# Kernel optimization log

Measured on AMD Instinct MI355X. Metric: run time of the kernel, lower is better.

The kernel has to match this reference:

```python
import jax, jax.numpy as jnp
import numpy as np

B, S, D, H = 2, 2048, 1024, 16
DK = D // H  # 64


def setup_inputs() -> dict:
    key = jax.random.key(0)
    k0, k1, k2, k3, k4, k5, k6 = jax.random.split(key, 7)
    scale = 0.02
    return {
        "q": jax.random.normal(k0, (B, S, D), dtype=jnp.float32),
        "k": jax.random.normal(k1, (B, S, D), dtype=jnp.float32),
        "v": jax.random.normal(k2, (B, S, D), dtype=jnp.float32),
        # per-head Q/K projection weights (n_head separate Linear layers, bias=False)
        "Wq": jax.random.normal(k3, (H, D, DK), dtype=jnp.float32) * scale,
        "Wk": jax.random.normal(k4, (H, D, DK), dtype=jnp.float32) * scale,
        # shared V projection (the same v_layer object is reused for every head)
        "Wv": jax.random.normal(k5, (D, DK), dtype=jnp.float32) * scale,
        # output projection fc: d_v -> d_model, bias=False
        "Wo": jax.random.normal(k6, (DK, D), dtype=jnp.float32) * scale,
    }


def reference(q, k, v, Wq, Wk, Wv, Wo):
    d_k = Wq.shape[-1]
    # batched per-head projections (replaces the Python loop over heads)
    qs = jnp.einsum("bsd,hdk->bhsk", q, Wq)          # [B,H,S,DK]
    ks = jnp.einsum("bsd,hdk->bhsk", k, Wk)          # [B,H,S,DK]
    vs = jnp.einsum("bsd,dk->bsk", v, Wv)            # [B,S,DK] shared across heads
    scores = jnp.einsum("bhsk,bhtk->bhst", qs, ks) / jnp.sqrt(
        jnp.asarray(d_k, dtype=jnp.float32)
    )                                                 # [B,H,S,S]
    attn = jax.nn.softmax(scores, axis=-1)            # [B,H,S,S]; dropout = identity (eval)
    heads = jnp.einsum("bhst,btk->bhsk", attn, vs)    # [B,H,S,DK]
    head = heads.mean(axis=1)                         # mean over heads, not concat
    attn_mean = attn.mean(axis=1)                     # [B,S,S]
    out = jnp.einsum("bsk,kd->bsd", head, Wo)         # [B,S,D]; dropout = identity
    return (out, attn_mean)
```

## Files before the change

kernel.cpp:

```cpp
#include <hip/hip_runtime.h>

#define B_ 2
#define S_ 2048
#define D_ 1024
#define H_ 16
#define DK_ 64

typedef __bf16 bf8 __attribute__((ext_vector_type(8)));
typedef float f4 __attribute__((ext_vector_type(4)));
typedef unsigned short u16x8 __attribute__((ext_vector_type(8)));

__device__ __forceinline__ unsigned short f2bf_bits(float f) {
  unsigned int u = __float_as_uint(f);
  return (unsigned short)((u + 0x7fffu + ((u >> 16) & 1u)) >> 16);
}

__device__ __forceinline__ bf8 pack_bf8(f4 lo, f4 hi) {
  u16x8 u;
  u[0] = f2bf_bits(lo[0]); u[1] = f2bf_bits(lo[1]);
  u[2] = f2bf_bits(lo[2]); u[3] = f2bf_bits(lo[3]);
  u[4] = f2bf_bits(hi[0]); u[5] = f2bf_bits(hi[1]);
  u[6] = f2bf_bits(hi[2]); u[7] = f2bf_bits(hi[3]);
  union { u16x8 u; bf8 b; } x; x.u = u; return x.b;
}

__device__ __forceinline__ bf8 ldb(const unsigned short* p) {
  return *reinterpret_cast<const bf8*>(p);
}

__device__ __forceinline__ void stage16(const void* g, void* l) {
  __builtin_amdgcn_global_load_lds(
      (const __attribute__((address_space(1))) void*)g,
      (__attribute__((address_space(3))) void*)l, 16, 0, 0);
}

#define MFMA(a, b, c) __builtin_amdgcn_mfma_f32_16x16x32_bf16((a), (b), (c), 0, 0, 0)

__global__ void k_prep(const float* __restrict__ q, const float* __restrict__ k,
                       const float* __restrict__ wq, const float* __restrict__ wk,
                       const float* __restrict__ wv, const float* __restrict__ wo,
                       unsigned short* __restrict__ qb, unsigned short* __restrict__ kb,
                       unsigned short* __restrict__ wqt, unsigned short* __restrict__ wkt,
                       unsigned short* __restrict__ wvt, unsigned short* __restrict__ wot) {
  int bid = blockIdx.x, tid = threadIdx.x;
  if (bid < 4096) {
    int which = bid >> 11;
    long i = ((long)(bid & 2047) * 256 + tid) * 8;
    const float* src = which ? k : q;
    unsigned short* dst = which ? kb : qb;
    f4 lo = *reinterpret_cast<const f4*>(src + i);
    f4 hi = *reinterpret_cast<const f4*>(src + i + 4);
    *reinterpret_cast<bf8*>(dst + i) = pack_bf8(lo, hi);
  } else if (bid < 8192) {
    int i = (bid - 4096) * 256 + tid;
    int h = i >> 16, rem = i & 65535, n = rem >> 10, d = rem & 1023;
    long src = ((long)h << 16) + d * 64 + n;
    wqt[i] = f2bf_bits(wq[src]);
    wkt[i] = f2bf_bits(wk[src]);
  } else {
    int i = (bid - 8192) * 256 + tid;
    int n = i >> 10, d = i & 1023;
    wvt[i] = f2bf_bits(wv[d * 64 + n]);
    int dd = i >> 6, kk = i & 63;
    wot[i] = f2bf_bits(wo[kk * 1024 + dd]);
  }
}

__global__ __launch_bounds__(256) void k_gemm_qk(
    const unsigned short* __restrict__ qb, const unsigned short* __restrict__ kb,
    const unsigned short* __restrict__ wqt, const unsigned short* __restrict__ wkt,
    unsigned short* __restrict__ qsb, unsigned short* __restrict__ ksb) {
  __shared__ unsigned short lds[6144];
  const int tid = threadIdx.x, wave = tid >> 6, lane = tid & 63;
  const int l15 = lane & 15, quad = lane >> 4;
  const int m0 = blockIdx.x * 128, n0 = blockIdx.y * 64;
  const int which = blockIdx.z;
  const unsigned short* A = which ? kb : qb;
  const unsigned short* W = which ? wkt : wqt;
  unsigned short* C = which ? ksb : qsb;
  const float scale = which ? 1.0f : 0.18033688011112042f;
  const int wr = wave >> 1, wc = wave & 1;

  f4 acc[4][2];
#pragma unroll
  for (int i = 0; i < 4; ++i)
#pragma unroll
    for (int j = 0; j < 2; ++j) acc[i][j] = f4{0.f, 0.f, 0.f, 0.f};

  const int sl15 = tid & 15, squad = (tid >> 4) & 3, sT = tid >> 6;

  for (int k0 = 0; k0 < D_; k0 += 32) {
    stage16(A + (long)(m0 + sT * 16 + sl15) * D_ + k0 + squad * 8, lds + tid * 8);
    stage16(A + (long)(m0 + 64 + sT * 16 + sl15) * D_ + k0 + squad * 8, lds + 2048 + tid * 8);
    stage16(W + (long)(n0 + sT * 16 + sl15) * D_ + k0 + squad * 8, lds + 4096 + tid * 8);
    __syncthreads();
    bf8 aF[4], bF[2];
#pragma unroll
    for (int mi = 0; mi < 4; ++mi)
      aF[mi] = ldb(lds + (wr * 4 + mi) * 512 + lane * 8);
#pragma unroll
    for (int ni = 0; ni < 2; ++ni)
      bF[ni] = ldb(lds + 4096 + (wc * 2 + ni) * 512 + lane * 8);
#pragma unroll
    for (int mi = 0; mi < 4; ++mi)
#pragma unroll
      for (int ni = 0; ni < 2; ++ni)
        acc[mi][ni] = MFMA(aF[mi], bF[ni], acc[mi][ni]);
    __syncthreads();
  }
#pragma unroll
  for (int mi = 0; mi < 4; ++mi)
#pragma unroll
    for (int r = 0; r < 4; ++r) {
      long row = m0 + wr * 64 + mi * 16 + quad * 4 + r;
#pragma unroll
      for (int ni = 0; ni < 2; ++ni)
        C[row * D_ + n0 + wc * 32 + ni * 16 + l15] = f2bf_bits(acc[mi][ni][r] * scale);
    }
}

__global__ __launch_bounds__(256) void k_pv(
    const float* __restrict__ v, const unsigned short* __restrict__ wvt,
    float* __restrict__ pv) {
  const int tid = threadIdx.x, wave = tid >> 6, lane = tid & 63;
  const int l15 = lane & 15, quad = lane >> 4;
  const int rg = blockIdx.x, kc = blockIdx.y;
  const int row0 = rg * 64 + wave * 16;
  const float* arow = v + (long)(row0 + l15) * D_ + kc * 256 + quad * 8;
  const unsigned short* wbase = wvt + kc * 256 + quad * 8;
  f4 acc[4];
  for (int i = 0; i < 4; ++i) acc[i] = f4{0.f, 0.f, 0.f, 0.f};
  for (int k0 = 0; k0 < 256; k0 += 32) {
    f4 alo = *reinterpret_cast<const f4*>(arow + k0);
    f4 ahi = *reinterpret_cast<const f4*>(arow + k0 + 4);
    bf8 a = pack_bf8(alo, ahi);
#pragma unroll
    for (int i = 0; i < 4; ++i) {
      bf8 bf = ldb(wbase + (long)(i * 16 + l15) * D_ + k0);
      acc[i] = MFMA(a, bf, acc[i]);
    }
  }
#pragma unroll
  for (int i = 0; i < 4; ++i)
#pragma unroll
    for (int r = 0; r < 4; ++r)
      pv[((long)kc * 4096 + row0 + quad * 4 + r) * 64 + i * 16 + l15] = acc[i][r];
}

__global__ void k_vred(const float* __restrict__ pv, unsigned short* __restrict__ vst) {
  int e = blockIdx.x * 256 + threadIdx.x;
  int t = e & 2047, dk = (e >> 11) & 63, b = e >> 17;
  long row = (long)b * S_ + t;
  float s = pv[row * 64 + dk] + pv[(4096 + row) * 64 + dk] +
            pv[(8192 + row) * 64 + dk] + pv[(12288 + row) * 64 + dk];
  vst[e] = f2bf_bits(s);
}

__global__ __launch_bounds__(1024) void k_denom(
    const unsigned short* __restrict__ qsb, const unsigned short* __restrict__ ksb,
    float* __restrict__ recip) {
  __shared__ unsigned short lds[8192];
  const int tid = threadIdx.x, wave = tid >> 6, lane = tid & 63;
  const int l15 = lane & 15, quad = lane >> 4;
  const int stile = blockIdx.x, h = blockIdx.y, b = blockIdx.z;
  const int s0 = stile * 256 + wave * 16;

  const unsigned short* qrow = qsb + ((long)(b * S_) + s0 + l15) * D_ + h * 64 + quad * 8;
  bf8 a0 = ldb(qrow);
  bf8 a1 = ldb(qrow + 32);

  const int sl15 = tid & 15, squad = (tid >> 4) & 3, stt = (tid >> 6) & 7, sh2 = tid >> 9;
  const unsigned short* gsrc0 =
      ksb + ((long)(b * S_) + stt * 16 + sl15) * D_ + h * 64 + sh2 * 32 + squad * 8;

  f4 sum = f4{0.f, 0.f, 0.f, 0.f};
  for (int t0 = 0; t0 < S_; t0 += 128) {
    stage16(gsrc0 + (long)t0 * D_, lds + tid * 8);
    __syncthreads();
#pragma unroll
    for (int tt = 0; tt < 8; ++tt) {
      bf8 b0 = ldb(lds + tt * 512 + lane * 8);
      bf8 b1 = ldb(lds + 4096 + tt * 512 + lane * 8);
      f4 d = f4{0.f, 0.f, 0.f, 0.f};
      d = MFMA(a0, b0, d);
      d = MFMA(a1, b1, d);
#pragma unroll
      for (int r = 0; r < 4; ++r) sum[r] += __builtin_amdgcn_exp2f(d[r]);
    }
    __syncthreads();
  }
#pragma unroll
  for (int m = 1; m < 16; m <<= 1) {
#pragma unroll
    for (int r = 0; r < 4; ++r) sum[r] += __shfl_xor(sum[r], m, 64);
  }
  if (l15 == 0) {
    float* rp = recip + (long)(b * H_ + h) * S_ + s0 + quad * 4;
#pragma unroll
    for (int r = 0; r < 4; ++r) rp[r] = 1.0f / (16.0f * sum[r]);
  }
}

__global__ __launch_bounds__(512) void k_attn(
    const unsigned short* __restrict__ qsb, const unsigned short* __restrict__ ksb,
    const float* __restrict__ recip, float* __restrict__ am) {
  __shared__ unsigned short lds[8192];
  const int tid = threadIdx.x, wave = tid >> 6, lane = tid & 63;
  const int l15 = lane & 15, quad = lane >> 4;
  const int tchunk = blockIdx.x, stile = blockIdx.y, b = blockIdx.z;
  const int s0 = stile * 128 + wave * 16;
  const int t0c = tchunk * 128;

  f4 acc[8];
#pragma unroll
  for (int tt = 0; tt < 8; ++tt) acc[tt] = f4{0.f, 0.f, 0.f, 0.f};

  const unsigned short* qbase = qsb + ((long)(b * S_) + s0 + l15) * D_ + quad * 8;

  for (int h = 0; h < H_; ++h) {
#pragma unroll
    for (int i = 0; i < 2; ++i) {
      int u = i * 512 + tid;
      int sl15 = u & 15, squad = (u >> 4) & 3, stt = (u >> 6) & 7, sh2 = u >> 9;
      stage16(ksb + ((long)(b * S_) + t0c + stt * 16 + sl15) * D_ + h * 64 + sh2 * 32 + squad * 8,
              lds + u * 8);
    }
    bf8 a0 = ldb(qbase + h * 64);
    bf8 a1 = ldb(qbase + h * 64 + 32);
    f4 rp = *reinterpret_cast<const f4*>(recip + (long)(b * H_ + h) * S_ + s0 + quad * 4);
    __syncthreads();
#pragma unroll
    for (int tt = 0; tt < 8; ++tt) {
      bf8 b0 = ldb(lds + tt * 512 + lane * 8);
      bf8 b1 = ldb(lds + 4096 + tt * 512 + lane * 8);
      f4 d = f4{0.f, 0.f, 0.f, 0.f};
      d = MFMA(a0, b0, d);
      d = MFMA(a1, b1, d);
#pragma unroll
      for (int r = 0; r < 4; ++r) acc[tt][r] += rp[r] * __builtin_amdgcn_exp2f(d[r]);
    }
    __syncthreads();
  }
  float* obase = am + ((long)b * S_ + s0 + quad * 4) * S_ + t0c + l15;
#pragma unroll
  for (int tt = 0; tt < 8; ++tt)
#pragma unroll
    for (int r = 0; r < 4; ++r) obase[(long)r * S_ + tt * 16] = acc[tt][r];
}

__global__ __launch_bounds__(256) void k_hpart(
    const float* __restrict__ am, const unsigned short* __restrict__ vst,
    float* __restrict__ ph) {
  const int tid = threadIdx.x, wave = tid >> 6, lane = tid & 63;
  const int l15 = lane & 15, quad = lane >> 4;
  const int rg = blockIdx.x, kc = blockIdx.y;
  const int row0 = rg * 64 + wave * 16;
  const int b = row0 >> 11;
  const float* arow = am + (long)(row0 + l15) * S_ + kc * 512 + quad * 8;
  const unsigned short* vb = vst + (long)b * DK_ * S_ + kc * 512 + quad * 8;
  f4 acc[4];
  for (int i = 0; i < 4; ++i) acc[i] = f4{0.f, 0.f, 0.f, 0.f};
  for (int t0 = 0; t0 < 512; t0 += 32) {
    f4 alo = *reinterpret_cast<const f4*>(arow + t0);
    f4 ahi = *reinterpret_cast<const f4*>(arow + t0 + 4);
    bf8 a = pack_bf8(alo, ahi);
#pragma unroll
    for (int i = 0; i < 4; ++i) {
      bf8 bf = ldb(vb + (long)(i * 16 + l15) * S_ + t0);
      acc[i] = MFMA(a, bf, acc[i]);
    }
  }
#pragma unroll
  for (int i = 0; i < 4; ++i)
#pragma unroll
    for (int r = 0; r < 4; ++r)
      ph[((long)kc * 4096 + row0 + quad * 4 + r) * 64 + i * 16 + l15] = acc[i][r];
}

__global__ void k_hred(const float* __restrict__ ph, unsigned short* __restrict__ headb) {
  int e = blockIdx.x * 256 + threadIdx.x;
  float s = ph[e] + ph[e + 4096 * 64] + ph[e + 2 * 4096 * 64] + ph[e + 3 * 4096 * 64];
  headb[e] = f2bf_bits(s);
}

__global__ __launch_bounds__(256) void k_out(
    const unsigned short* __restrict__ head, const unsigned short* __restrict__ wot,
    float* __restrict__ out) {
  const int tid = threadIdx.x, wave = tid >> 6, lane = tid & 63;
  const int l15 = lane & 15, quad = lane >> 4;
  const int dchunk = blockIdx.x, stile = blockIdx.y, b = blockIdx.z;
  const int s0 = stile * 64 + wave * 16;
  const int n0 = dchunk * 128;
  const unsigned short* hrow = head + ((long)b * S_ + s0 + l15) * DK_ + quad * 8;
  bf8 a0 = ldb(hrow);
  bf8 a1 = ldb(hrow + 32);
  const unsigned short* wb = wot + quad * 8;
  float* obase = out + ((long)b * S_ + s0 + quad * 4) * D_ + n0 + l15;
#pragma unroll
  for (int i = 0; i < 8; ++i) {
    const unsigned short* wp = wb + (long)(n0 + i * 16 + l15) * DK_;
    bf8 b0 = ldb(wp);
    bf8 b1 = ldb(wp + 32);
    f4 d = f4{0.f, 0.f, 0.f, 0.f};
    d = MFMA(a0, b0, d);
    d = MFMA(a1, b1, d);
#pragma unroll
    for (int r = 0; r < 4; ++r) obase[(long)r * D_ + i * 16] = d[r];
  }
}

extern "C" void kernel_launch(void* const* d_in, const int* in_sizes, int n_in,
                              void* d_out, int out_size, void* d_ws, size_t ws_size,
                              hipStream_t stream) {
  const float* q  = (const float*)d_in[0];
  const float* k  = (const float*)d_in[1];
  const float* v  = (const float*)d_in[2];
  const float* Wq = (const float*)d_in[3];
  const float* Wk = (const float*)d_in[4];
  const float* Wv = (const float*)d_in[5];
  const float* Wo = (const float*)d_in[6];

  float* out = (float*)d_out;
  float* am  = out + (long)B_ * S_ * D_;

  unsigned short* qsb  = (unsigned short*)d_ws;
  unsigned short* ksb  = qsb + 4194304;
  unsigned short* wqt  = ksb + 4194304;
  unsigned short* wkt  = wqt + 1048576;
  unsigned short* wvt  = wkt + 1048576;
  unsigned short* wot  = wvt + 65536;
  unsigned short* vst  = wot + 65536;
  unsigned short* headb= vst + 262144;
  float* recip = (float*)(headb + 262144);

  unsigned short* qb = (unsigned short*)am;
  unsigned short* kb = qb + 4194304;
  float* part = out;

  k_prep<<<8448, 256, 0, stream>>>(q, k, Wq, Wk, Wv, Wo, qb, kb, wqt, wkt, wvt, wot);
  k_gemm_qk<<<dim3(32, 16, 2), 256, 0, stream>>>(qb, kb, wqt, wkt, qsb, ksb);
  k_pv<<<dim3(64, 4), 256, 0, stream>>>(v, wvt, part);
  k_vred<<<1024, 256, 0, stream>>>(part, vst);
  k_denom<<<dim3(8, 16, 2), 1024, 0, stream>>>(qsb, ksb, recip);
  k_attn<<<dim3(16, 16, 2), 512, 0, stream>>>(qsb, ksb, recip, am);
  k_hpart<<<dim3(64, 4), 256, 0, stream>>>(am, vst, part);
  k_hred<<<1024, 256, 0, stream>>>(part, headb);
  k_out<<<dim3(8, 32, 2), 256, 0, stream>>>(headb, wot, out);
}
```

Baseline: 266.1 us.

## Tile weight transposes via LDS, widen QK GEMM tile, halve denom block size

The weight transpose-and-convert in the prep kernel now goes through a padded 64x64 LDS tile, so both its global reads and writes are coalesced instead of strided, and the prep grid shrinks accordingly. The Q/K projection GEMM tile grows from 128x64 to 128x128 per block, doubling the MFMA work per staged A tile and cutting redundant A loads. The softmax-denominator kernel moves from 1024-thread to 512-thread blocks, each covering 128 rows and staging K with two loads per thread, which doubles the grid. Risks include more accumulator registers in the GEMM and fewer GEMM blocks to fill the device.

```diff
diff --git a/kernel.cpp b/kernel.cpp
--- a/kernel.cpp
+++ b/kernel.cpp
@@ -42,7 +42,9 @@
                        unsigned short* __restrict__ qb, unsigned short* __restrict__ kb,
                        unsigned short* __restrict__ wqt, unsigned short* __restrict__ wkt,
                        unsigned short* __restrict__ wvt, unsigned short* __restrict__ wot) {
+  __shared__ float tl[64 * 65];
   int bid = blockIdx.x, tid = threadIdx.x;
+  const int rr = tid >> 6, cc = tid & 63;
   if (bid < 4096) {
     int which = bid >> 11;
     long i = ((long)(bid & 2047) * 256 + tid) * 8;
@@ -51,18 +53,51 @@
     f4 lo = *reinterpret_cast<const f4*>(src + i);
     f4 hi = *reinterpret_cast<const f4*>(src + i + 4);
     *reinterpret_cast<bf8*>(dst + i) = pack_bf8(lo, hi);
-  } else if (bid < 8192) {
-    int i = (bid - 4096) * 256 + tid;
-    int h = i >> 16, rem = i & 65535, n = rem >> 10, d = rem & 1023;
-    long src = ((long)h << 16) + d * 64 + n;
-    wqt[i] = f2bf_bits(wq[src]);
-    wkt[i] = f2bf_bits(wk[src]);
+  } else if (bid < 4352) {
+    int blk = bid - 4096;
+    int h = blk >> 4, d0 = (blk & 15) * 64;
+    for (int m = 0; m < 2; ++m) {
+      const float* src = m ? wk : wq;
+      unsigned short* dst = m ? wkt : wqt;
+      if (m) __syncthreads();
+#pragma unroll
+      for (int it = 0; it < 16; ++it) {
+        int d = it * 4 + rr;
+        tl[cc * 65 + d] = src[(long)h * 65536 + (d0 + d) * 64 + cc];
+      }
+      __syncthreads();
+#pragma unroll
+      for (int it = 0; it < 16; ++it) {
+        int n = it * 4 + rr;
+        dst[(long)h * 65536 + n * 1024 + d0 + cc] = f2bf_bits(tl[n * 65 + cc]);
+      }
+    }
+  } else if (bid < 4368) {
+    int d0 = (bid - 4352) * 64;
+#pragma unroll
+    for (int it = 0; it < 16; ++it) {
+      int d = it * 4 + rr;
+      tl[cc * 65 + d] = wv[(long)(d0 + d) * 64 + cc];
+    }
+    __syncthreads();
+#pragma unroll
+    for (int it = 0; it < 16; ++it) {
+      int n = it * 4 + rr;
+      wvt[(long)n * 1024 + d0 + cc] = f2bf_bits(tl[n * 65 + cc]);
+    }
   } else {
-    int i = (bid - 8192) * 256 + tid;
-    int n = i >> 10, d = i & 1023;
-    wvt[i] = f2bf_bits(wv[d * 64 + n]);
-    int dd = i >> 6, kk = i & 63;
-    wot[i] = f2bf_bits(wo[kk * 1024 + dd]);
+    int d0 = (bid - 4368) * 64;
+#pragma unroll
+    for (int it = 0; it < 16; ++it) {
+      int kk = it * 4 + rr;
+      tl[cc * 65 + kk] = wo[(long)kk * 1024 + d0 + cc];
+    }
+    __syncthreads();
+#pragma unroll
+    for (int it = 0; it < 16; ++it) {
+      int ddl = it * 4 + rr;
+      wot[(long)(d0 + ddl) * 64 + cc] = f2bf_bits(tl[ddl * 65 + cc]);
+    }
   }
 }
 
@@ -70,10 +105,10 @@
     const unsigned short* __restrict__ qb, const unsigned short* __restrict__ kb,
     const unsigned short* __restrict__ wqt, const unsigned short* __restrict__ wkt,
     unsigned short* __restrict__ qsb, unsigned short* __restrict__ ksb) {
-  __shared__ unsigned short lds[6144];
-  const int tid = threadIdx.x, wave = tid >> 6, lane = tid & 63;
-  const int l15 = lane & 15, quad = lane >> 4;
-  const int m0 = blockIdx.x * 128, n0 = blockIdx.y * 64;
+  __shared__ unsigned short lds[8192];
+  const int tid = threadIdx.x, wave = tid >> 6, lane = tid & 63;
+  const int l15 = lane & 15, quad = lane >> 4;
+  const int m0 = blockIdx.x * 128, n0 = blockIdx.y * 128;
   const int which = blockIdx.z;
   const unsigned short* A = which ? kb : qb;
   const unsigned short* W = which ? wkt : wqt;
@@ -81,30 +116,33 @@
   const float scale = which ? 1.0f : 0.18033688011112042f;
   const int wr = wave >> 1, wc = wave & 1;
 
-  f4 acc[4][2];
+  f4 acc[4][4];
 #pragma unroll
   for (int i = 0; i < 4; ++i)
 #pragma unroll
-    for (int j = 0; j < 2; ++j) acc[i][j] = f4{0.f, 0.f, 0.f, 0.f};
-
-  const int sl15 = tid & 15, squad = (tid >> 4) & 3, sT = tid >> 6;
+    for (int j = 0; j < 4; ++j) acc[i][j] = f4{0.f, 0.f, 0.f, 0.f};
+
+  const int sl15 = tid & 15, squad = (tid >> 4) & 3, st = tid >> 6;
+  const unsigned short* gA = A + (long)(m0 + st * 16 + sl15) * D_ + squad * 8;
+  const unsigned short* gB = W + (long)(n0 + st * 16 + sl15) * D_ + squad * 8;
 
   for (int k0 = 0; k0 < D_; k0 += 32) {
-    stage16(A + (long)(m0 + sT * 16 + sl15) * D_ + k0 + squad * 8, lds + tid * 8);
-    stage16(A + (long)(m0 + 64 + sT * 16 + sl15) * D_ + k0 + squad * 8, lds + 2048 + tid * 8);
-    stage16(W + (long)(n0 + sT * 16 + sl15) * D_ + k0 + squad * 8, lds + 4096 + tid * 8);
-    __syncthreads();
-    bf8 aF[4], bF[2];
+    stage16(gA + k0, lds + tid * 8);
+    stage16(gA + 64 * D_ + k0, lds + 2048 + tid * 8);
+    stage16(gB + k0, lds + 4096 + tid * 8);
+    stage16(gB + 64 * D_ + k0, lds + 6144 + tid * 8);
+    __syncthreads();
+    bf8 aF[4], bF[4];
 #pragma unroll
     for (int mi = 0; mi < 4; ++mi)
       aF[mi] = ldb(lds + (wr * 4 + mi) * 512 + lane * 8);
 #pragma unroll
-    for (int ni = 0; ni < 2; ++ni)
-      bF[ni] = ldb(lds + 4096 + (wc * 2 + ni) * 512 + lane * 8);
+    for (int ni = 0; ni < 4; ++ni)
+      bF[ni] = ldb(lds + 4096 + (wc * 4 + ni) * 512 + lane * 8);
 #pragma unroll
     for (int mi = 0; mi < 4; ++mi)
 #pragma unroll
-      for (int ni = 0; ni < 2; ++ni)
+      for (int ni = 0; ni < 4; ++ni)
         acc[mi][ni] = MFMA(aF[mi], bF[ni], acc[mi][ni]);
     __syncthreads();
   }
@@ -114,8 +152,8 @@
     for (int r = 0; r < 4; ++r) {
       long row = m0 + wr * 64 + mi * 16 + quad * 4 + r;
 #pragma unroll
-      for (int ni = 0; ni < 2; ++ni)
-        C[row * D_ + n0 + wc * 32 + ni * 16 + l15] = f2bf_bits(acc[mi][ni][r] * scale);
+      for (int ni = 0; ni < 4; ++ni)
+        C[row * D_ + n0 + wc * 64 + ni * 16 + l15] = f2bf_bits(acc[mi][ni][r] * scale);
     }
 }
 
@@ -156,26 +194,28 @@
   vst[e] = f2bf_bits(s);
 }
 
-__global__ __launch_bounds__(1024) void k_denom(
+__global__ __launch_bounds__(512) void k_denom(
     const unsigned short* __restrict__ qsb, const unsigned short* __restrict__ ksb,
     float* __restrict__ recip) {
   __shared__ unsigned short lds[8192];
   const int tid = threadIdx.x, wave = tid >> 6, lane = tid & 63;
   const int l15 = lane & 15, quad = lane >> 4;
   const int stile = blockIdx.x, h = blockIdx.y, b = blockIdx.z;
-  const int s0 = stile * 256 + wave * 16;
+  const int s0 = stile * 128 + wave * 16;
 
   const unsigned short* qrow = qsb + ((long)(b * S_) + s0 + l15) * D_ + h * 64 + quad * 8;
   bf8 a0 = ldb(qrow);
   bf8 a1 = ldb(qrow + 32);
 
-  const int sl15 = tid & 15, squad = (tid >> 4) & 3, stt = (tid >> 6) & 7, sh2 = tid >> 9;
-  const unsigned short* gsrc0 =
-      ksb + ((long)(b * S_) + stt * 16 + sl15) * D_ + h * 64 + sh2 * 32 + squad * 8;
-
   f4 sum = f4{0.f, 0.f, 0.f, 0.f};
   for (int t0 = 0; t0 < S_; t0 += 128) {
-    stage16(gsrc0 + (long)t0 * D_, lds + tid * 8);
+#pragma unroll
+    for (int i = 0; i < 2; ++i) {
+      int u = i * 512 + tid;
+      int sl15 = u & 15, squad = (u >> 4) & 3, stt = (u >> 6) & 7, sh2 = u >> 9;
+      stage16(ksb + ((long)(b * S_) + t0 + stt * 16 + sl15) * D_ + h * 64 + sh2 * 32 + squad * 8,
+              lds + u * 8);
+    }
     __syncthreads();
 #pragma unroll
     for (int tt = 0; tt < 8; ++tt) {
@@ -337,11 +377,11 @@
   unsigned short* kb = qb + 4194304;
   float* part = out;
 
-  k_prep<<<8448, 256, 0, stream>>>(q, k, Wq, Wk, Wv, Wo, qb, kb, wqt, wkt, wvt, wot);
-  k_gemm_qk<<<dim3(32, 16, 2), 256, 0, stream>>>(qb, kb, wqt, wkt, qsb, ksb);
+  k_prep<<<4384, 256, 0, stream>>>(q, k, Wq, Wk, Wv, Wo, qb, kb, wqt, wkt, wvt, wot);
+  k_gemm_qk<<<dim3(32, 8, 2), 256, 0, stream>>>(qb, kb, wqt, wkt, qsb, ksb);
   k_pv<<<dim3(64, 4), 256, 0, stream>>>(v, wvt, part);
   k_vred<<<1024, 256, 0, stream>>>(part, vst);
-  k_denom<<<dim3(8, 16, 2), 1024, 0, stream>>>(qsb, ksb, recip);
+  k_denom<<<dim3(16, 16, 2), 512, 0, stream>>>(qsb, ksb, recip);
   k_attn<<<dim3(16, 16, 2), 512, 0, stream>>>(qsb, ksb, recip, am);
   k_hpart<<<dim3(64, 4), 256, 0, stream>>>(am, vst, part);
   k_hred<<<1024, 256, 0, stream>>>(part, headb);
```

Result: faster. 246.9 us (-7.2%).
